# Performance work log

Hardware: AMD Instinct MI355X
Metric: run time of the kernel (lower is better)

## Reference

```python
import jax, jax.numpy as jnp
import numpy as np

N_HEAD = 8


def setup_inputs() -> dict:
    key = jax.random.key(0)
    k1, k2, k3, k4 = jax.random.split(key, 4)
    B, C, T, F = 2, 128, 512, 512
    x = jax.random.normal(k1, (B, C, T, F), dtype=jnp.float32)
    Wq = jax.random.normal(k2, (F, F), dtype=jnp.float32) * (F ** -0.5)
    bq = jax.random.normal(k3, (F,), dtype=jnp.float32) * 0.02
    Wk = jax.random.normal(k4, (F, F), dtype=jnp.float32) * (F ** -0.5)
    return {"x": x, "Wq": Wq, "bq": bq, "Wk": Wk}


def reference(x, Wq, bq, Wk):
    B, C, T, F = x.shape
    H = N_HEAD
    d = F // H
    # v: permute (0,1,3,2) -> (B,C,F,T), flatten -> (B,C,F*T)
    v = jnp.transpose(x, (0, 1, 3, 2)).reshape(B, C, F * T)
    # mean over permuted dim 3 (== original T axis)
    xm = jnp.mean(x, axis=2)  # (B,C,F)
    q = xm @ Wq.T + bq        # (B,C,F)
    k = xm @ Wk.T             # (B,C,F)
    scale = d ** (-0.25)
    qh = q.reshape(B, C, H, d).transpose(0, 2, 1, 3) * scale   # (B,H,C,d)
    kh = k.reshape(B, C, H, d).transpose(0, 2, 3, 1) * scale   # (B,H,d,C)
    dv = (F * T) // H
    vh = v.reshape(B, C, H, dv).transpose(0, 2, 1, 3)          # (B,H,C,dv)
    qk = jnp.einsum('bhcd,bhdk->bhck', qh, kh)                 # (B,H,C,C)
    w = jax.nn.softmax(qk.astype(jnp.float32), axis=-1).astype(qh.dtype)
    wv = jnp.einsum('bhck,bhkd->bhcd', w, vh)                  # (B,H,C,dv)
    wv = wv.transpose(0, 2, 1, 3).reshape(B, C, F * T).reshape(B, C, F, T)
    # inverse permute (0,1,3,2) -> (B,C,T,F)
    return jnp.transpose(wv, (0, 1, 3, 2))
```

## Files before the change

kernel.cpp:

```cpp
#include <hip/hip_runtime.h>
#include <hip/hip_bf16.h>

#define BB 2
#define CC 128
#define TT 512
#define FF 512
#define HH 8

typedef __attribute__((ext_vector_type(8))) short short8;
typedef __attribute__((ext_vector_type(4))) float f32x4;

__device__ __forceinline__ unsigned short f2b(float f) {
    union { float f; unsigned u; } a; a.f = f;
    unsigned r = a.u + 0x7fffu + ((a.u >> 16) & 1u);
    return (unsigned short)(r >> 16);
}

__global__ void mean_kernel(const float* __restrict__ x, float* __restrict__ xm) {
    int bc = blockIdx.x;
    int q4  = threadIdx.x & 127;
    int par = threadIdx.x >> 7;
    const float4* xp = (const float4*)(x + (size_t)bc * (TT * FF));
    float4 s = make_float4(0.f, 0.f, 0.f, 0.f);
    #pragma unroll 8
    for (int t = par; t < TT; t += 2) {
        float4 v = xp[t * 128 + q4];
        s.x += v.x; s.y += v.y; s.z += v.z; s.w += v.w;
    }
    __shared__ float4 part[256];
    part[threadIdx.x] = s;
    __syncthreads();
    if (par == 0) {
        float4 o = part[threadIdx.x + 128];
        const float inv = 1.0f / (float)TT;
        s.x = (s.x + o.x) * inv; s.y = (s.y + o.y) * inv;
        s.z = (s.z + o.z) * inv; s.w = (s.w + o.w) * inv;
        ((float4*)xm)[bc * 128 + q4] = s;
    }
}

__global__ void qk_kernel(const float* __restrict__ xm, const float* __restrict__ Wq,
                          const float* __restrict__ bq, const float* __restrict__ Wk,
                          float* __restrict__ qo, float* __restrict__ ko) {
    __shared__ float xs[32][65];
    __shared__ float wqs[32][65];
    __shared__ float wks[32][65];
    int ft = blockIdx.x, rt = blockIdx.y;
    int t = threadIdx.x;
    int tx = t & 15, ty = t >> 4;
    float qa[2][2] = {{0.f,0.f},{0.f,0.f}}, ka[2][2] = {{0.f,0.f},{0.f,0.f}};
    for (int kc = 0; kc < 512; kc += 64) {
        __syncthreads();
        for (int i = t; i < 2048; i += 256) {
            int r = i >> 6, cc2 = i & 63;
            xs[r][cc2]  = xm[(rt * 32 + r) * 512 + kc + cc2];
            wqs[r][cc2] = Wq[(ft * 32 + r) * 512 + kc + cc2];
            wks[r][cc2] = Wk[(ft * 32 + r) * 512 + kc + cc2];
        }
        __syncthreads();
        #pragma unroll 8
        for (int kk = 0; kk < 64; ++kk) {
            float x0 = xs[ty*2][kk],  x1 = xs[ty*2+1][kk];
            float a0 = wqs[tx*2][kk], a1 = wqs[tx*2+1][kk];
            float b0 = wks[tx*2][kk], b1 = wks[tx*2+1][kk];
            qa[0][0] += x0*a0; qa[0][1] += x0*a1;
            qa[1][0] += x1*a0; qa[1][1] += x1*a1;
            ka[0][0] += x0*b0; ka[0][1] += x0*b1;
            ka[1][0] += x1*b0; ka[1][1] += x1*b1;
        }
    }
    #pragma unroll
    for (int i = 0; i < 2; ++i) {
        int r = rt * 32 + ty * 2 + i;
        #pragma unroll
        for (int j = 0; j < 2; ++j) {
            int f = ft * 32 + tx * 2 + j;
            qo[r * 512 + f] = qa[i][j] + bq[f];
            ko[r * 512 + f] = ka[i][j];
        }
    }
}

__global__ void attn_w_kernel(const float* __restrict__ q, const float* __restrict__ k,
                              float* __restrict__ w) {
    int idx = blockIdx.x;
    int bh = idx >> 7, c = idx & 127;
    int b = bh >> 3, h = bh & 7;
    int f0 = h * 64;
    __shared__ float qv[64];
    __shared__ float wmax[2];
    __shared__ float wsum[2];
    int t = threadIdx.x;
    if (t < 64) qv[t] = q[((b * CC + c) * FF) + f0 + t];
    __syncthreads();
    const float* kp = k + ((size_t)(b * CC + t) * FF) + f0;
    float acc = 0.f;
    #pragma unroll
    for (int j = 0; j < 64; j += 4) {
        float4 kv = *(const float4*)(kp + j);
        acc += qv[j] * kv.x + qv[j+1] * kv.y + qv[j+2] * kv.z + qv[j+3] * kv.w;
    }
    float logit = acc * 0.125f;
    float m = logit;
    #pragma unroll
    for (int o = 32; o >= 1; o >>= 1) m = fmaxf(m, __shfl_xor(m, o));
    if ((t & 63) == 0) wmax[t >> 6] = m;
    __syncthreads();
    m = fmaxf(wmax[0], wmax[1]);
    float e = expf(logit - m);
    float s = e;
    #pragma unroll
    for (int o = 32; o >= 1; o >>= 1) s += __shfl_xor(s, o);
    if ((t & 63) == 0) wsum[t >> 6] = s;
    __syncthreads();
    s = wsum[0] + wsum[1];
    w[((size_t)bh * 128 + c) * 128 + t] = e / s;
}

__global__ __launch_bounds__(256, 2) void wv_kernel(const float* __restrict__ x,
                                                    const float* __restrict__ wmat,
                                                    float* __restrict__ out) {
    constexpr int CS = TT * FF;
    int bh = blockIdx.y;
    int b = bh >> 3, h = bh & 7;
    __shared__ unsigned short Wl[128 * 128];

    {
        int t = threadIdx.x;
        int c = t >> 1;
        int half = (t & 1) << 6;
        const float* wp = wmat + ((size_t)bh * 128 + c) * 128 + half;
        unsigned swz = (unsigned)((c & 7) << 4);
        char* base = (char*)Wl + c * 256;
        #pragma unroll
        for (int i = 0; i < 64; i += 4) {
            float4 v = *(const float4*)(wp + i);
            unsigned p0 = (unsigned)f2b(v.x) | ((unsigned)f2b(v.y) << 16);
            unsigned p1 = (unsigned)f2b(v.z) | ((unsigned)f2b(v.w) << 16);
            unsigned e2 = (unsigned)((half + i) << 1);
            *(unsigned*)(base + ((e2     ) ^ swz)) = p0;
            *(unsigned*)(base + ((e2 + 4u) ^ swz)) = p1;
        }
    }
    __syncthreads();

    int ln  = threadIdx.x & 63;
    int wv_ = threadIdx.x >> 6;
    int nco = ln & 15;
    int kg  = ln >> 4;
    int arow = ln & 15;
    unsigned aswz = (unsigned)((arow & 7) << 4);
    const float* xb = x + (size_t)b * CC * CS;
    float* ob = out + (size_t)b * CC * CS;

    for (int it = 0; it < 8; ++it) {
        int ti = blockIdx.x * 4 + wv_ + it * 128;
        int col0 = ti << 5;
        int t = col0 >> 6;
        int fbase = (h << 6) + (col0 & 63);
        const float* xc = xb + (size_t)t * FF + fbase + nco + (size_t)(kg * 8) * CS;

        f32x4 acc[8][2];
        #pragma unroll
        for (int m = 0; m < 8; ++m) {
            acc[m][0] = (f32x4){0.f, 0.f, 0.f, 0.f};
            acc[m][1] = (f32x4){0.f, 0.f, 0.f, 0.f};
        }

        #pragma unroll
        for (int ks = 0; ks < 4; ++ks) {
            const float* p0 = xc + (size_t)(ks * 32) * CS;
            short8 bf[2];
            #pragma unroll
            for (int nt = 0; nt < 2; ++nt) {
                const float* p = p0 + nt * 16;
                float v0 = p[0];
                float v1 = p[(size_t)1 * CS];
                float v2 = p[(size_t)2 * CS];
                float v3 = p[(size_t)3 * CS];
                float v4 = p[(size_t)4 * CS];
                float v5 = p[(size_t)5 * CS];
                float v6 = p[(size_t)6 * CS];
                float v7 = p[(size_t)7 * CS];
                short8 bb;
                bb[0] = (short)f2b(v0); bb[1] = (short)f2b(v1);
                bb[2] = (short)f2b(v2); bb[3] = (short)f2b(v3);
                bb[4] = (short)f2b(v4); bb[5] = (short)f2b(v5);
                bb[6] = (short)f2b(v6); bb[7] = (short)f2b(v7);
                bf[nt] = bb;
            }
            #pragma unroll
            for (int m = 0; m < 8; ++m) {
                unsigned abyte = (unsigned)((m * 16 + arow) * 256)
                               + (((unsigned)((ks * 4 + kg) << 4)) ^ aswz);
                short8 af = *(const short8*)((const char*)Wl + abyte);
                acc[m][0] = __builtin_amdgcn_mfma_f32_16x16x32_bf16(af, bf[0], acc[m][0], 0, 0, 0);
                acc[m][1] = __builtin_amdgcn_mfma_f32_16x16x32_bf16(af, bf[1], acc[m][1], 0, 0, 0);
            }
        }

        float* o0 = ob + (size_t)t * FF + fbase + nco;
        #pragma unroll
        for (int m = 0; m < 8; ++m) {
            int crow = m * 16 + kg * 4;
            #pragma unroll
            for (int nt = 0; nt < 2; ++nt) {
                float* op = o0 + (size_t)crow * CS + nt * 16;
                #pragma unroll
                for (int j = 0; j < 4; ++j) {
                    op[(size_t)j * CS] = acc[m][nt][j];
                }
            }
        }
    }
}

extern "C" void kernel_launch(void* const* d_in, const int* in_sizes, int n_in,
                              void* d_out, int out_size, void* d_ws, size_t ws_size,
                              hipStream_t stream) {
    (void)in_sizes; (void)n_in; (void)out_size; (void)ws_size;
    const float* x  = (const float*)d_in[0];
    const float* Wq = (const float*)d_in[1];
    const float* bq = (const float*)d_in[2];
    const float* Wk = (const float*)d_in[3];
    float* out = (float*)d_out;

    float* ws = (float*)d_ws;
    float* xm = ws;
    float* q  = ws + 131072;
    float* k  = ws + 262144;
    float* w  = ws + 393216;

    hipLaunchKernelGGL(mean_kernel,   dim3(256),     dim3(256), 0, stream, x, xm);
    hipLaunchKernelGGL(qk_kernel,     dim3(16, 8),   dim3(256), 0, stream, xm, Wq, bq, Wk, q, k);
    hipLaunchKernelGGL(attn_w_kernel, dim3(2048),    dim3(128), 0, stream, q, k, w);
    hipLaunchKernelGGL(wv_kernel,     dim3(32, 16),  dim3(256), 0, stream, x, w, out);
}
```

Measured before the change: 237.9 us.

## Widen mean kernel blocks and restructure wv kernel for higher occupancy

The mean reduction now uses 1024 threads per block, with two independent accumulators per thread and an 8-way shared-memory combine, to raise memory-level parallelism. The wv kernel loads and converts all B fragments up front, then computes one output row-tile at a time with two accumulators. This drops the 64-register accumulator array, so launch bounds can rise to 4 blocks per CU and the grid doubles to 64x16. The aim is more waves in flight to hide HBM latency, at the cost of more blocks each staging the 32KB W matrix into LDS again, and stores that are interleaved with MFMAs.

```diff
diff --git a/kernel.cpp b/kernel.cpp
--- a/kernel.cpp
+++ b/kernel.cpp
@@ -16,26 +16,34 @@
     return (unsigned short)(r >> 16);
 }
 
-__global__ void mean_kernel(const float* __restrict__ x, float* __restrict__ xm) {
+__global__ __launch_bounds__(1024) void mean_kernel(const float* __restrict__ x,
+                                                    float* __restrict__ xm) {
     int bc = blockIdx.x;
     int q4  = threadIdx.x & 127;
     int par = threadIdx.x >> 7;
     const float4* xp = (const float4*)(x + (size_t)bc * (TT * FF));
-    float4 s = make_float4(0.f, 0.f, 0.f, 0.f);
-    #pragma unroll 8
-    for (int t = par; t < TT; t += 2) {
-        float4 v = xp[t * 128 + q4];
-        s.x += v.x; s.y += v.y; s.z += v.z; s.w += v.w;
-    }
-    __shared__ float4 part[256];
-    part[threadIdx.x] = s;
+    float4 s0 = make_float4(0.f,0.f,0.f,0.f), s1 = make_float4(0.f,0.f,0.f,0.f);
+    #pragma unroll 4
+    for (int k = 0; k < 64; k += 2) {
+        float4 a = xp[(par + 8 * k) * 128 + q4];
+        float4 b = xp[(par + 8 * (k + 1)) * 128 + q4];
+        s0.x += a.x; s0.y += a.y; s0.z += a.z; s0.w += a.w;
+        s1.x += b.x; s1.y += b.y; s1.z += b.z; s1.w += b.w;
+    }
+    s0.x += s1.x; s0.y += s1.y; s0.z += s1.z; s0.w += s1.w;
+    __shared__ float4 part[1024];
+    part[threadIdx.x] = s0;
     __syncthreads();
     if (par == 0) {
-        float4 o = part[threadIdx.x + 128];
         const float inv = 1.0f / (float)TT;
-        s.x = (s.x + o.x) * inv; s.y = (s.y + o.y) * inv;
-        s.z = (s.z + o.z) * inv; s.w = (s.w + o.w) * inv;
-        ((float4*)xm)[bc * 128 + q4] = s;
+        float4 acc = make_float4(0.f,0.f,0.f,0.f);
+        #pragma unroll
+        for (int j = 0; j < 8; ++j) {
+            float4 v = part[q4 + 128 * j];
+            acc.x += v.x; acc.y += v.y; acc.z += v.z; acc.w += v.w;
+        }
+        acc.x *= inv; acc.y *= inv; acc.z *= inv; acc.w *= inv;
+        ((float4*)xm)[bc * 128 + q4] = acc;
     }
 }
 
@@ -117,7 +125,7 @@
     w[((size_t)bh * 128 + c) * 128 + t] = e / s;
 }
 
-__global__ __launch_bounds__(256, 2) void wv_kernel(const float* __restrict__ x,
+__global__ __launch_bounds__(256, 4) void wv_kernel(const float* __restrict__ x,
                                                     const float* __restrict__ wmat,
                                                     float* __restrict__ out) {
     constexpr int CS = TT * FF;
@@ -153,63 +161,47 @@
     const float* xb = x + (size_t)b * CC * CS;
     float* ob = out + (size_t)b * CC * CS;
 
-    for (int it = 0; it < 8; ++it) {
-        int ti = blockIdx.x * 4 + wv_ + it * 128;
+    for (int it = 0; it < 4; ++it) {
+        int ti = blockIdx.x * 4 + wv_ + it * 256;
         int col0 = ti << 5;
         int t = col0 >> 6;
         int fbase = (h << 6) + (col0 & 63);
         const float* xc = xb + (size_t)t * FF + fbase + nco + (size_t)(kg * 8) * CS;
 
-        f32x4 acc[8][2];
-        #pragma unroll
-        for (int m = 0; m < 8; ++m) {
-            acc[m][0] = (f32x4){0.f, 0.f, 0.f, 0.f};
-            acc[m][1] = (f32x4){0.f, 0.f, 0.f, 0.f};
-        }
-
+        short8 bf[4][2];
         #pragma unroll
         for (int ks = 0; ks < 4; ++ks) {
             const float* p0 = xc + (size_t)(ks * 32) * CS;
-            short8 bf[2];
             #pragma unroll
             for (int nt = 0; nt < 2; ++nt) {
                 const float* p = p0 + nt * 16;
-                float v0 = p[0];
-                float v1 = p[(size_t)1 * CS];
-                float v2 = p[(size_t)2 * CS];
-                float v3 = p[(size_t)3 * CS];
-                float v4 = p[(size_t)4 * CS];
-                float v5 = p[(size_t)5 * CS];
-                float v6 = p[(size_t)6 * CS];
-                float v7 = p[(size_t)7 * CS];
                 short8 bb;
-                bb[0] = (short)f2b(v0); bb[1] = (short)f2b(v1);
-                bb[2] = (short)f2b(v2); bb[3] = (short)f2b(v3);
-                bb[4] = (short)f2b(v4); bb[5] = (short)f2b(v5);
-                bb[6] = (short)f2b(v6); bb[7] = (short)f2b(v7);
-                bf[nt] = bb;
+                #pragma unroll
+                for (int j = 0; j < 8; ++j) bb[j] = (short)f2b(p[(size_t)j * CS]);
+                bf[ks][nt] = bb;
             }
+        }
+
+        float* o0 = ob + (size_t)t * FF + fbase + nco;
+        #pragma unroll
+        for (int m = 0; m < 8; ++m) {
+            f32x4 acc0 = (f32x4){0.f,0.f,0.f,0.f};
+            f32x4 acc1 = (f32x4){0.f,0.f,0.f,0.f};
             #pragma unroll
-            for (int m = 0; m < 8; ++m) {
+            for (int ks = 0; ks < 4; ++ks) {
                 unsigned abyte = (unsigned)((m * 16 + arow) * 256)
                                + (((unsigned)((ks * 4 + kg) << 4)) ^ aswz);
                 short8 af = *(const short8*)((const char*)Wl + abyte);
-                acc[m][0] = __builtin_amdgcn_mfma_f32_16x16x32_bf16(af, bf[0], acc[m][0], 0, 0, 0);
-                acc[m][1] = __builtin_amdgcn_mfma_f32_16x16x32_bf16(af, bf[1], acc[m][1], 0, 0, 0);
+                acc0 = __builtin_amdgcn_mfma_f32_16x16x32_bf16(af, bf[ks][0], acc0, 0, 0, 0);
+                acc1 = __builtin_amdgcn_mfma_f32_16x16x32_bf16(af, bf[ks][1], acc1, 0, 0, 0);
             }
-        }
-
-        float* o0 = ob + (size_t)t * FF + fbase + nco;
-        #pragma unroll
-        for (int m = 0; m < 8; ++m) {
             int crow = m * 16 + kg * 4;
+            float* op0 = o0 + (size_t)crow * CS;
+            float* op1 = op0 + 16;
             #pragma unroll
-            for (int nt = 0; nt < 2; ++nt) {
-                float* op = o0 + (size_t)crow * CS + nt * 16;
-                #pragma unroll
-                for (int j = 0; j < 4; ++j) {
-                    op[(size_t)j * CS] = acc[m][nt][j];
-                }
+            for (int j = 0; j < 4; ++j) {
+                op0[(size_t)j * CS] = acc0[j];
+                op1[(size_t)j * CS] = acc1[j];
             }
         }
     }
@@ -231,8 +223,8 @@
     float* k  = ws + 262144;
     float* w  = ws + 393216;
 
-    hipLaunchKernelGGL(mean_kernel,   dim3(256),     dim3(256), 0, stream, x, xm);
-    hipLaunchKernelGGL(qk_kernel,     dim3(16, 8),   dim3(256), 0, stream, xm, Wq, bq, Wk, q, k);
-    hipLaunchKernelGGL(attn_w_kernel, dim3(2048),    dim3(128), 0, stream, q, k, w);
-    hipLaunchKernelGGL(wv_kernel,     dim3(32, 16),  dim3(256), 0, stream, x, w, out);
-}
+    hipLaunchKernelGGL(mean_kernel,   dim3(256),     dim3(1024), 0, stream, x, xm);
+    hipLaunchKernelGGL(qk_kernel,     dim3(16, 8),   dim3(256),  0, stream, xm, Wq, bq, Wk, q, k);
+    hipLaunchKernelGGL(attn_w_kernel, dim3(2048),    dim3(128),  0, stream, q, k, w);
+    hipLaunchKernelGGL(wv_kernel,     dim3(64, 16),  dim3(256),  0, stream, x, w, out);
+}
```

Result: slower. 293.8 us (+23.5%).
